# Kernel optimization log

Measured on AMD Instinct MI355X. Metric: run time of the kernel, lower is better.

## Reference

```python
import jax, jax.numpy as jnp
import numpy as np

GRID_SIZE = 8
SPLINE_ORDER = 3
GRID_LO, GRID_HI = -1.0, 1.0
EPS = 1e-5  # InstanceNorm2d default eps
C = 16
K = GRID_SIZE + SPLINE_ORDER  # number of B-spline basis channels per input channel


def make_grid():
    h = (GRID_HI - GRID_LO) / GRID_SIZE
    # extended knot vector, length grid_size + 2*spline_order + 1
    return jnp.arange(-SPLINE_ORDER, GRID_SIZE + SPLINE_ORDER + 1, dtype=jnp.float32) * h + GRID_LO


def bspline_bases(x, grid):
    # x: [B,C,H,W] -> bases: [B,C,H,W,K] via Cox-de Boor recursion
    xu = x[..., None]
    bases = ((xu >= grid[:-1]) & (xu < grid[1:])).astype(x.dtype)
    for k in range(1, SPLINE_ORDER + 1):
        left = grid[:-(k + 1)]
        right = grid[k:-1]
        delta = jnp.where(right == left, jnp.ones_like(right), right - left)
        bases = ((xu - left) / delta) * bases[..., :-1] + \
                ((grid[k + 1:] - xu) / (grid[k + 1:] - grid[1:-k])) * bases[..., 1:]
    return bases


def conv2d(x, w):
    # NCHW conv, stride 1, padding 1 (kernel 3x3), bias=False as in KANConv2DLayer
    return jax.lax.conv_general_dilated(
        x, w, window_strides=(1, 1), padding=[(1, 1), (1, 1)],
        dimension_numbers=('NCHW', 'OIHW', 'NCHW'))


def instance_norm(x):
    # nn.InstanceNorm2d(affine=False): normalize over H,W per (N,C)
    m = jnp.mean(x, axis=(2, 3), keepdims=True)
    v = jnp.var(x, axis=(2, 3), keepdims=True)
    return (x - m) * jax.lax.rsqrt(v + EPS)


def prelu(x, a):
    return jnp.where(x >= 0, x, a * x)


def kan_conv_layer(x, base_w, spline_w, prelu_a, grid):
    base_out = conv2d(jax.nn.silu(x), base_w)
    b = bspline_bases(x, grid)                      # [B,C,H,W,K]
    B, Cx, H, W, Kx = b.shape
    b = jnp.moveaxis(b, -1, 2).reshape(B, Cx * Kx, H, W)
    spline_out = conv2d(b, spline_w)
    return prelu(instance_norm(base_out + spline_out), prelu_a)


def setup_inputs() -> dict:
    key = jax.random.key(0)
    ks = jax.random.split(key, 5)
    s = 0.05
    return {
        'x': jax.random.normal(ks[0], (4, C, 512, 512), jnp.float32),
        'base_w1': jax.random.normal(ks[1], (C, C, 3, 3), jnp.float32) * s,
        'spline_w1': jax.random.normal(ks[2], (C, C * K, 3, 3), jnp.float32) * s,
        'prelu_a1': jnp.float32(0.25),
        'base_w2': jax.random.normal(ks[3], (C, C, 3, 3), jnp.float32) * s,
        'spline_w2': jax.random.normal(ks[4], (C, C * K, 3, 3), jnp.float32) * s,
        'prelu_a2': jnp.float32(0.25),
    }


def reference(x, base_w1, spline_w1, prelu_a1, base_w2, spline_w2, prelu_a2):
    grid = make_grid()
    y = kan_conv_layer(x, base_w1, spline_w1, prelu_a1, grid)
    y = kan_conv_layer(y, base_w2, spline_w2, prelu_a2, grid)
    return jax.nn.sigmoid(y)
```

## Files before the change

kernel.cpp:

```cpp
#include <hip/hip_runtime.h>
#include <cstddef>
#include <cstdint>

#define HW    512
#define CCH   16
#define TR    12
#define HTILE 18
#define HTR   14
#define NPIX2 252
#define NSLOT 12

typedef _Float16 f16x8 __attribute__((ext_vector_type(8)));
typedef float    f32x4 __attribute__((ext_vector_type(4)));

__device__ __forceinline__ float h2f(ushort u) {
    _Float16 h = __builtin_bit_cast(_Float16, u);
    return (float)h;
}
__device__ __forceinline__ ushort f2h(float f) {
    _Float16 h = (_Float16)f;
    return __builtin_bit_cast(ushort, h);
}
__device__ __forceinline__ uint pack2h(float a, float b) {
    return (uint)f2h(a) | ((uint)f2h(b) << 16);
}

__device__ __forceinline__ void derived12(float x, uint* u) {
    float si = x / (1.0f + __expf(-x));
    float t  = fmaf(x, 4.0f, 7.0f);
    t = fminf(fmaxf(t, -1.0f), 15.0f);
    float ft = floorf(t);
    int   ci = (int)ft;
    float uu = t - ft;
    float um = 1.0f - uu;
    float u2 = uu * uu, m2 = um * um;
    float u3 = u2 * uu, m3 = m2 * um;
    const float c16 = 0.16666667f, c23 = 0.66666667f;
    float w0 = u3 * c16;
    float w3 = m3 * c16;
    float w2 = fmaf(0.5f, u3, c23 - u2);
    float w1 = fmaf(0.5f, m3, c23 - m2);
    uint64_t P = (uint64_t)f2h(w3)
               | ((uint64_t)f2h(w2) << 16)
               | ((uint64_t)f2h(w1) << 32)
               | ((uint64_t)f2h(w0) << 48);
    int s = 16 * ci - 48;
    int d = s >> 6;
    int e = s & 63;
    uint64_t Q = P << e;
    uint64_t R = (P >> (63 - e)) >> 1;
    uint64_t O0 = (d == 0) ? Q : (d == -1) ? R : 0ull;
    uint64_t O1 = (d == 1) ? Q : (d ==  0) ? R : 0ull;
    uint64_t O2 = (d == 2) ? Q : (d ==  1) ? R : 0ull;
    O2 = (O2 & 0x0000ffffffffffffull) | ((uint64_t)f2h(si) << 48);
    u[0] = (uint)O0; u[1] = (uint)(O0 >> 32);
    u[2] = (uint)O1; u[3] = (uint)(O1 >> 32);
    u[4] = (uint)O2; u[5] = (uint)(O2 >> 32);
}

__global__ void __launch_bounds__(64) prep_w(
    const float* __restrict__ bw1, const float* __restrict__ sw1,
    const float* __restrict__ bw2, const float* __restrict__ sw2,
    uint4* __restrict__ wtab1, uint4* __restrict__ wtab2,
    float* __restrict__ part1, float* __restrict__ part2)
{
    const int s    = blockIdx.x;
    const int lane = threadIdx.x;
    const float* bw; const float* sw; uint4* wt;
    if (blockIdx.y == 0) { bw = bw1; sw = sw1; wt = wtab1; }
    else                 { bw = bw2; sw = sw2; wt = wtab2; }

    if (s == 0) {
        float* p = (blockIdx.y == 0) ? part1 : part2;
        p[lane] = 0.0f;
        p[64 + lane] = 0.0f;
    }

    const int co = lane & 15, q = lane >> 4;
    const int chunk = s / 27, sl = s - chunk * 27;
    uint u[4];
#pragma unroll
    for (int jj = 0; jj < 4; ++jj) {
        float w[2];
#pragma unroll
        for (int h = 0; h < 2; ++h) {
            int j   = jj * 2 + h;
            int kl  = 32 * sl + 8 * q + j;
            int tap = kl / 96;
            int r   = kl - tap * 96;
            int ci  = r / 12;
            int kv  = r - ci * 12;
            int cin = chunk * 8 + ci;
            w[h] = (kv == 11) ? bw[(co * 16 + cin) * 9 + tap]
                              : sw[(co * 176 + cin * 11 + kv) * 9 + tap];
        }
        u[jj] = pack2h(w[0], w[1]);
    }
    wt[s * 64 + lane] = make_uint4(u[0], u[1], u[2], u[3]);
}

template<bool IN_H, bool OUT_H, bool NORM_IN>
__global__ __launch_bounds__(256, 3) void conv_mfma(
    const void* __restrict__ in_v,
    const uint4* __restrict__ wtab,
    void* __restrict__ out_v,
    const float* __restrict__ stats_in,
    const float* __restrict__ a_in,
    float* __restrict__ part_out)
{
    __shared__ uint4 dt16[NSLOT * NPIX2];
    __shared__ float sn[32];

    const int tid  = threadIdx.x;
    const int lane = tid & 63;
    const int wv   = tid >> 6;
    const int m    = lane & 15;
    const int q    = lane >> 4;
    const int bx0  = blockIdx.x * 16;
    const int by0  = blockIdx.y * TR;
    const int b    = blockIdx.z;

    const float*  inf = (const float*)in_v;
    const ushort* inh = (const ushort*)in_v;

    float pa = 0.0f;
    if (NORM_IN) {
        pa = *a_in;
        if (tid < 32) sn[tid] = stats_in[b * 32 + tid];
    }

    bool livek[2], okk[2];
    int  cbk[2];
    uint yxk[2], bok[2];
#pragma unroll
    for (int k = 0; k < 2; ++k) {
        int it  = tid + k * 256;
        bool lv = it < 2 * NPIX2;
        int cpg = (it >= NPIX2) ? 1 : 0;
        int pix = it - cpg * NPIX2;
        int py  = pix / HTILE;
        int px  = pix - py * HTILE;
        int gy  = by0 + py - 1;
        int gx  = bx0 + px - 1;
        livek[k] = lv;
        okk[k]   = lv && ((unsigned)gy < (unsigned)HW)
                      && ((unsigned)gx < (unsigned)HW);
        cbk[k]   = cpg * 4;
        yxk[k]   = ((uint)gy << 9) + (uint)gx;
        bok[k]   = (uint)(cpg * 6 * NPIX2 + pix);
    }

#define STAGE_LOADS(CHUNK, V) do {                                           \
    _Pragma("unroll")                                                        \
    for (int k_ = 0; k_ < 2; ++k_) {                                         \
        _Pragma("unroll")                                                    \
        for (int c_ = 0; c_ < 4; ++c_) {                                     \
            float x_ = -1.0e9f;                 \
            if (okk[k_]) {                                                   \
                size_t base_ = ((size_t)(b * CCH + (CHUNK) * 8               \
                               + cbk[k_] + c_) << 18) + yxk[k_];             \
                if (IN_H) x_ = h2f(inh[base_]);                              \
                else      x_ = inf[base_];                                   \
            }                                                                \
            (V)[k_ * 4 + c_] = x_;                                           \
        }                                                                    \
    } } while (0)

#define DERIVE_WRITE(CHUNK, V) do {                                          \
    _Pragma("unroll")                                                        \
    for (int k_ = 0; k_ < 2; ++k_) {                                         \
        if (livek[k_]) {                                                     \
            _Pragma("unroll")                                                \
            for (int pr_ = 0; pr_ < 2; ++pr_) {                              \
                float a0_ = (V)[k_ * 4 + pr_ * 2];                           \
                float c0_ = (V)[k_ * 4 + pr_ * 2 + 1];                       \
                if (NORM_IN) {                                               \
                    int ci2_ = ((CHUNK) * 8 + cbk[k_] + pr_ * 2) * 2;        \
                    a0_ = (a0_ - sn[ci2_])     * sn[ci2_ + 1];               \
                    a0_ = (a0_ >= 0.f) ? a0_ : pa * a0_;                     \
                    c0_ = (c0_ - sn[ci2_ + 2]) * sn[ci2_ + 3];               \
                    c0_ = (c0_ >= 0.f) ? c0_ : pa * c0_;                     \
                }                                                            \
                uint uA_[6], uB_[6];                                         \
                derived12(a0_, uA_);                                         \
                derived12(c0_, uB_);                                         \
                uint bo_ = bok[k_] + (uint)(pr_ * 3 * NPIX2);                \
                dt16[bo_]             = make_uint4(uA_[0], uA_[1], uA_[2], uA_[3]); \
                dt16[bo_ + NPIX2]     = make_uint4(uA_[4], uA_[5], uB_[0], uB_[1]); \
                dt16[bo_ + 2 * NPIX2] = make_uint4(uB_[2], uB_[3], uB_[4], uB_[5]); \
            }                                                                \
        }                                                                    \
    } } while (0)

#define KLOOP(CHUNK) do {                                                    \
    uint4 wf_[27];                                                           \
    _Pragma("unroll")                                                        \
    for (int s_ = 0; s_ < 27; ++s_)                                          \
        wf_[s_] = wtab[((CHUNK) * 27 + s_) * 64 + lane];                     \
    const uint pixbase_ = (uint)(wv * 3 * HTILE + m);                        \
    _Pragma("unroll")                                                        \
    for (int j_ = 0; j_ < 3; ++j_) {                                         \
        const uint slotoff_ = (uint)((j_ * 4 + q) * NPIX2) + pixbase_;       \
        _Pragma("unroll")                                                    \
        for (int tdx_ = 0; tdx_ < 3; ++tdx_) {                               \
            f16x8 brow_[5];                                                  \
            _Pragma("unroll")                                                \
            for (int r6_ = 0; r6_ < 5; ++r6_)                                \
                brow_[r6_] = *reinterpret_cast<const f16x8*>(                \
                    &dt16[slotoff_ + (uint)(r6_ * HTILE + tdx_)]);           \
            _Pragma("unroll")                                                \
            for (int tdy_ = 0; tdy_ < 3; ++tdy_) {                           \
                const int s_ = (tdy_ * 3 + tdx_) * 3 + j_;                   \
                _Pragma("unroll")                                            \
                for (int t_ = 0; t_ < 3; ++t_)                               \
                    acc[t_] = __builtin_amdgcn_mfma_f32_16x16x32_f16(        \
                        __builtin_bit_cast(f16x8, wf_[s_]),                  \
                        brow_[t_ + tdy_], acc[t_], 0, 0, 0);                 \
            }                                                                \
        }                                                                    \
    } } while (0)

    f32x4 acc[3];
#pragma unroll
    for (int t = 0; t < 3; ++t) acc[t] = f32x4{0.f, 0.f, 0.f, 0.f};

    float va[8], vb[8];

    STAGE_LOADS(0, va);
    __syncthreads();
    DERIVE_WRITE(0, va);
    __syncthreads();
    STAGE_LOADS(1, vb);
    KLOOP(0);
    __syncthreads();
    DERIVE_WRITE(1, vb);
    __syncthreads();
    KLOOP(1);

#pragma unroll
    for (int t = 0; t < 3; ++t) {
        int oy = by0 + wv * 3 + t;
        if (oy < HW) {
#pragma unroll
            for (int r = 0; r < 4; ++r) {
                int co = q * 4 + r;
                size_t idx = ((size_t)(b * CCH + co) << 18)
                           + ((size_t)oy << 9) + (bx0 + m);
                if (OUT_H) ((ushort*)out_v)[idx] = f2h(acc[t][r]);
                else       ((float*)out_v)[idx]  = acc[t][r];
            }
        }
    }

    float s4[4], q4[4];
#pragma unroll
    for (int r = 0; r < 4; ++r) { s4[r] = 0.0f; q4[r] = 0.0f; }
#pragma unroll
    for (int t = 0; t < 3; ++t) {
        int oy = by0 + wv * 3 + t;
        if (oy < HW) {
#pragma unroll
            for (int r = 0; r < 4; ++r) {
                s4[r] += acc[t][r];
                q4[r] = fmaf(acc[t][r], acc[t][r], q4[r]);
            }
        }
    }
#pragma unroll
    for (int off = 8; off > 0; off >>= 1) {
#pragma unroll
        for (int r = 0; r < 4; ++r) {
            s4[r] += __shfl_xor(s4[r], off);
            q4[r] += __shfl_xor(q4[r], off);
        }
    }
    __syncthreads();
    float* scr = (float*)dt16;
    if (m == 0) {
#pragma unroll
        for (int r = 0; r < 4; ++r) {
            scr[(wv * 16 + q * 4 + r) * 2 + 0] = s4[r];
            scr[(wv * 16 + q * 4 + r) * 2 + 1] = q4[r];
        }
    }
    __syncthreads();
    if (tid < 32) {
        int co = tid >> 1, which = tid & 1;
        float v = scr[(0 * 16 + co) * 2 + which] + scr[(1 * 16 + co) * 2 + which]
                + scr[(2 * 16 + co) * 2 + which] + scr[(3 * 16 + co) * 2 + which];
        atomicAdd(&part_out[(size_t)(b * CCH + co) * 2 + which], v);
    }
#undef STAGE_LOADS
#undef DERIVE_WRITE
#undef KLOOP
}

__global__ void __launch_bounds__(64) reduce_final(
    const float* __restrict__ part, float* __restrict__ stats)
{
    const int bc = threadIdx.x;
    const float inv = 1.0f / 262144.0f;
    float s  = part[bc * 2];
    float qq = part[bc * 2 + 1];
    float mval = s * inv;
    float var  = qq * inv - mval * mval;
    stats[bc * 2]     = mval;
    stats[bc * 2 + 1] = rsqrtf(var + 1e-5f);
}

__global__ void __launch_bounds__(256) final_sigmoid(
    float* __restrict__ out, const float* __restrict__ stats,
    const float* __restrict__ a_ptr)
{
    const float a = *a_ptr;
    const int i4 = blockIdx.x * 256 + threadIdx.x;
    const int bc = i4 >> 16;
    const float mm = stats[bc * 2];
    const float rr = stats[bc * 2 + 1];
    float4 v = reinterpret_cast<float4*>(out)[i4];
    float t;
    t = (v.x - mm) * rr; t = (t >= 0.f) ? t : a * t; v.x = 1.0f / (1.0f + __expf(-t));
    t = (v.y - mm) * rr; t = (t >= 0.f) ? t : a * t; v.y = 1.0f / (1.0f + __expf(-t));
    t = (v.z - mm) * rr; t = (t >= 0.f) ? t : a * t; v.z = 1.0f / (1.0f + __expf(-t));
    t = (v.w - mm) * rr; t = (t >= 0.f) ? t : a * t; v.w = 1.0f / (1.0f + __expf(-t));
    reinterpret_cast<float4*>(out)[i4] = v;
}

extern "C" void kernel_launch(void* const* d_in, const int* in_sizes, int n_in,
                              void* d_out, int out_size, void* d_ws, size_t ws_size,
                              hipStream_t stream)
{
    const float* x        = (const float*)d_in[0];
    const float* base_w1  = (const float*)d_in[1];
    const float* spline_w1= (const float*)d_in[2];
    const float* prelu_a1 = (const float*)d_in[3];
    const float* base_w2  = (const float*)d_in[4];
    const float* spline_w2= (const float*)d_in[5];
    const float* prelu_a2 = (const float*)d_in[6];
    float* out_f = (float*)d_out;
    char*  wsb   = (char*)d_ws;

    ushort* z1h    = (ushort*)wsb;
    uint4*  wtab1  = (uint4*)(wsb + 33554432);
    uint4*  wtab2  = (uint4*)(wsb + 33609728);
    float*  part1  = (float*)(wsb + 33665024);
    float*  part2  = (float*)(wsb + 33665536);
    float*  stats1 = (float*)(wsb + 33666048);
    float*  stats2 = (float*)(wsb + 33666560);

    dim3 cgrid(HW / 16, (HW + TR - 1) / TR, 4);
    dim3 cblk(256);

    prep_w<<<dim3(54, 2), 64, 0, stream>>>(base_w1, spline_w1, base_w2, spline_w2,
                                           wtab1, wtab2, part1, part2);

    conv_mfma<false, true, false><<<cgrid, cblk, 0, stream>>>(
        x, wtab1, z1h, nullptr, nullptr, part1);
    reduce_final<<<1, 64, 0, stream>>>(part1, stats1);

    conv_mfma<true, false, true><<<cgrid, cblk, 0, stream>>>(
        z1h, wtab2, out_f, stats1, prelu_a1, part2);
    reduce_final<<<1, 64, 0, stream>>>(part2, stats2);

    final_sigmoid<<<16384, cblk, 0, stream>>>(out_f, stats2, prelu_a2);
}
```

Measured before the change: 415.2 us.

## Enlarge conv tile to 16x16 rows per block with four row accumulators

Each block's output tile grows from 12 to 16 rows, so each wave computes 4 output rows instead of 3. The halo overhead per output pixel drops (18x18 halo for 16x16 outputs versus 18x14 for 12x16) and the grid now divides 512 evenly, which removes the bounds checks on rows. The cost is more LDS per block and more registers, so launch bounds drop from 3 to 2 blocks per CU, lowering occupancy. The change also raises wave priority around the MFMA loop with s_setprio.

```diff
diff --git a/kernel.cpp b/kernel.cpp
--- a/kernel.cpp
+++ b/kernel.cpp
@@ -4,10 +4,8 @@
 
 #define HW    512
 #define CCH   16
-#define TR    12
 #define HTILE 18
-#define HTR   14
-#define NPIX2 252
+#define NPIX  324
 #define NSLOT 12
 
 typedef _Float16 f16x8 __attribute__((ext_vector_type(8)));
@@ -100,7 +98,7 @@
 }
 
 template<bool IN_H, bool OUT_H, bool NORM_IN>
-__global__ __launch_bounds__(256, 3) void conv_mfma(
+__global__ __launch_bounds__(256, 2) void conv_mfma(
     const void* __restrict__ in_v,
     const uint4* __restrict__ wtab,
     void* __restrict__ out_v,
@@ -108,7 +106,7 @@
     const float* __restrict__ a_in,
     float* __restrict__ part_out)
 {
-    __shared__ uint4 dt16[NSLOT * NPIX2];
+    __shared__ uint4 dt16[NSLOT * NPIX];
     __shared__ float sn[32];
 
     const int tid  = threadIdx.x;
@@ -117,7 +115,7 @@
     const int m    = lane & 15;
     const int q    = lane >> 4;
     const int bx0  = blockIdx.x * 16;
-    const int by0  = blockIdx.y * TR;
+    const int by0  = blockIdx.y * 16;
     const int b    = blockIdx.z;
 
     const float*  inf = (const float*)in_v;
@@ -129,15 +127,16 @@
         if (tid < 32) sn[tid] = stats_in[b * 32 + tid];
     }
 
-    bool livek[2], okk[2];
-    int  cbk[2];
-    uint yxk[2], bok[2];
-#pragma unroll
-    for (int k = 0; k < 2; ++k) {
+    bool livek[3], okk[3];
+    int  cbk[3];
+    uint yxk[3], bok[3];
+#pragma unroll
+    for (int k = 0; k < 3; ++k) {
         int it  = tid + k * 256;
-        bool lv = it < 2 * NPIX2;
-        int cpg = (it >= NPIX2) ? 1 : 0;
-        int pix = it - cpg * NPIX2;
+        bool lv = it < 2 * NPIX;
+        int cpg = (it >= NPIX) ? 1 : 0;
+        int pix = it - cpg * NPIX;
+        if (!lv) pix = 0;
         int py  = pix / HTILE;
         int px  = pix - py * HTILE;
         int gy  = by0 + py - 1;
@@ -147,12 +146,12 @@
                       && ((unsigned)gx < (unsigned)HW);
         cbk[k]   = cpg * 4;
         yxk[k]   = ((uint)gy << 9) + (uint)gx;
-        bok[k]   = (uint)(cpg * 6 * NPIX2 + pix);
+        bok[k]   = (uint)(cpg * 6 * NPIX + pix);
     }
 
 #define STAGE_LOADS(CHUNK, V) do {                                           \
     _Pragma("unroll")                                                        \
-    for (int k_ = 0; k_ < 2; ++k_) {                                         \
+    for (int k_ = 0; k_ < 3; ++k_) {                                         \
         _Pragma("unroll")                                                    \
         for (int c_ = 0; c_ < 4; ++c_) {                                     \
             float x_ = -1.0e9f;                 \
@@ -168,7 +167,7 @@
 
 #define DERIVE_WRITE(CHUNK, V) do {                                          \
     _Pragma("unroll")                                                        \
-    for (int k_ = 0; k_ < 2; ++k_) {                                         \
+    for (int k_ = 0; k_ < 3; ++k_) {                                         \
         if (livek[k_]) {                                                     \
             _Pragma("unroll")                                                \
             for (int pr_ = 0; pr_ < 2; ++pr_) {                              \
@@ -184,10 +183,10 @@
                 uint uA_[6], uB_[6];                                         \
                 derived12(a0_, uA_);                                         \
                 derived12(c0_, uB_);                                         \
-                uint bo_ = bok[k_] + (uint)(pr_ * 3 * NPIX2);                \
-                dt16[bo_]             = make_uint4(uA_[0], uA_[1], uA_[2], uA_[3]); \
-                dt16[bo_ + NPIX2]     = make_uint4(uA_[4], uA_[5], uB_[0], uB_[1]); \
-                dt16[bo_ + 2 * NPIX2] = make_uint4(uB_[2], uB_[3], uB_[4], uB_[5]); \
+                uint bo_ = bok[k_] + (uint)(pr_ * 3 * NPIX);                 \
+                dt16[bo_]            = make_uint4(uA_[0], uA_[1], uA_[2], uA_[3]); \
+                dt16[bo_ + NPIX]     = make_uint4(uA_[4], uA_[5], uB_[0], uB_[1]); \
+                dt16[bo_ + 2 * NPIX] = make_uint4(uB_[2], uB_[3], uB_[4], uB_[5]); \
             }                                                                \
         }                                                                    \
     } } while (0)
@@ -197,34 +196,37 @@
     _Pragma("unroll")                                                        \
     for (int s_ = 0; s_ < 27; ++s_)                                          \
         wf_[s_] = wtab[((CHUNK) * 27 + s_) * 64 + lane];                     \
-    const uint pixbase_ = (uint)(wv * 3 * HTILE + m);                        \
+    const uint pixbase_ = (uint)(wv * 4 * HTILE + m);                        \
+    __builtin_amdgcn_s_setprio(1);                                           \
     _Pragma("unroll")                                                        \
     for (int j_ = 0; j_ < 3; ++j_) {                                         \
-        const uint slotoff_ = (uint)((j_ * 4 + q) * NPIX2) + pixbase_;       \
+        const uint slotoff_ = (uint)((j_ * 4 + q) * NPIX) + pixbase_;        \
         _Pragma("unroll")                                                    \
         for (int tdx_ = 0; tdx_ < 3; ++tdx_) {                               \
-            f16x8 brow_[5];                                                  \
+            f16x8 brow_[6];                                                  \
             _Pragma("unroll")                                                \
-            for (int r6_ = 0; r6_ < 5; ++r6_)                                \
+            for (int r6_ = 0; r6_ < 6; ++r6_)                                \
                 brow_[r6_] = *reinterpret_cast<const f16x8*>(                \
                     &dt16[slotoff_ + (uint)(r6_ * HTILE + tdx_)]);           \
             _Pragma("unroll")                                                \
             for (int tdy_ = 0; tdy_ < 3; ++tdy_) {                           \
                 const int s_ = (tdy_ * 3 + tdx_) * 3 + j_;                   \
                 _Pragma("unroll")                                            \
-                for (int t_ = 0; t_ < 3; ++t_)                               \
+                for (int t_ = 0; t_ < 4; ++t_)                               \
                     acc[t_] = __builtin_amdgcn_mfma_f32_16x16x32_f16(        \
                         __builtin_bit_cast(f16x8, wf_[s_]),                  \
                         brow_[t_ + tdy_], acc[t_], 0, 0, 0);                 \
             }                                                                \
         }                                                                    \
-    } } while (0)
-
-    f32x4 acc[3];
-#pragma unroll
-    for (int t = 0; t < 3; ++t) acc[t] = f32x4{0.f, 0.f, 0.f, 0.f};
-
-    float va[8], vb[8];
+    }                                                                        \
+    __builtin_amdgcn_s_setprio(0);                                           \
+    } while (0)
+
+    f32x4 acc[4];
+#pragma unroll
+    for (int t = 0; t < 4; ++t) acc[t] = f32x4{0.f, 0.f, 0.f, 0.f};
+
+    float va[12], vb[12];
 
     STAGE_LOADS(0, va);
     __syncthreads();
@@ -238,33 +240,25 @@
     KLOOP(1);
 
 #pragma unroll
-    for (int t = 0; t < 3; ++t) {
-        int oy = by0 + wv * 3 + t;
-        if (oy < HW) {
-#pragma unroll
-            for (int r = 0; r < 4; ++r) {
-                int co = q * 4 + r;
-                size_t idx = ((size_t)(b * CCH + co) << 18)
-                           + ((size_t)oy << 9) + (bx0 + m);
-                if (OUT_H) ((ushort*)out_v)[idx] = f2h(acc[t][r]);
-                else       ((float*)out_v)[idx]  = acc[t][r];
-            }
+    for (int t = 0; t < 4; ++t) {
+        int oy = by0 + wv * 4 + t;
+#pragma unroll
+        for (int r = 0; r < 4; ++r) {
+            int co = q * 4 + r;
+            size_t idx = ((size_t)(b * CCH + co) << 18)
+                       + ((size_t)oy << 9) + (bx0 + m);
+            if (OUT_H) ((ushort*)out_v)[idx] = f2h(acc[t][r]);
+            else       ((float*)out_v)[idx]  = acc[t][r];
         }
     }
 
     float s4[4], q4[4];
 #pragma unroll
-    for (int r = 0; r < 4; ++r) { s4[r] = 0.0f; q4[r] = 0.0f; }
-#pragma unroll
-    for (int t = 0; t < 3; ++t) {
-        int oy = by0 + wv * 3 + t;
-        if (oy < HW) {
-#pragma unroll
-            for (int r = 0; r < 4; ++r) {
-                s4[r] += acc[t][r];
-                q4[r] = fmaf(acc[t][r], acc[t][r], q4[r]);
-            }
-        }
+    for (int r = 0; r < 4; ++r) {
+        s4[r] = acc[0][r] + acc[1][r] + acc[2][r] + acc[3][r];
+        q4[r] = fmaf(acc[0][r], acc[0][r],
+                fmaf(acc[1][r], acc[1][r],
+                fmaf(acc[2][r], acc[2][r], acc[3][r] * acc[3][r])));
     }
 #pragma unroll
     for (int off = 8; off > 0; off >>= 1) {
@@ -348,7 +342,7 @@
     float*  stats1 = (float*)(wsb + 33666048);
     float*  stats2 = (float*)(wsb + 33666560);
 
-    dim3 cgrid(HW / 16, (HW + TR - 1) / TR, 4);
+    dim3 cgrid(HW / 16, HW / 16, 4);
     dim3 cblk(256);
 
     prep_w<<<dim3(54, 2), 64, 0, stream>>>(base_w1, spline_w1, base_w2, spline_w2,
```

Result: faster. 390.1 us (-6.1%).
